# Kernel optimization log

Hardware: AMD Instinct MI355X
Metric: run time of the kernel (lower is better)

The kernel has to match this reference:

```python
import jax, jax.numpy as jnp
import numpy as np

SYM_LIST = np.array([0, 2, 5], dtype=np.int64)


def quat_to_rot_wxyz(q):
    """q: [bs, 4] normalized quaternion in wxyz order -> [bs, 3, 3] rotation."""
    w, x, y, z = q[:, 0], q[:, 1], q[:, 2], q[:, 3]
    two = jnp.asarray(2.0, q.dtype)
    one = jnp.asarray(1.0, q.dtype)
    r00 = one - two * (y * y + z * z)
    r01 = two * (x * y - z * w)
    r02 = two * (x * z + y * w)
    r10 = two * (x * y + z * w)
    r11 = one - two * (x * x + z * z)
    r12 = two * (y * z - x * w)
    r20 = two * (x * z - y * w)
    r21 = two * (y * z + x * w)
    r22 = one - two * (x * x + y * y)
    R = jnp.stack([
        jnp.stack([r00, r01, r02], axis=-1),
        jnp.stack([r10, r11, r12], axis=-1),
        jnp.stack([r20, r21, r22], axis=-1),
    ], axis=-2)  # [bs, 3, 3]
    return R


def setup_inputs() -> dict:
    key = jax.random.key(0)
    k1, k2, k3, k4, k5 = jax.random.split(key, 5)
    bs, num_p = 32, 2048
    pred_r = jax.random.normal(k1, (bs, 4), dtype=jnp.float32)
    pred_t = jax.random.normal(k2, (bs, 3), dtype=jnp.float32)
    target = jax.random.normal(k3, (bs, num_p, 3), dtype=jnp.float32)
    model_points = jax.random.normal(k4, (bs, num_p, 3), dtype=jnp.float32)
    idx = jax.random.randint(k5, (bs, 1), 0, 8, dtype=jnp.int64)
    return {"pred_r": pred_r, "pred_t": pred_t, "target": target,
            "model_points": model_points, "idx": idx, "permutation": 0}


def reference(pred_r, pred_t, target, model_points, idx, permutation):
    # normalize quaternion, build rotation, transform model points (row-vector
    # convention as in torch.bmm(model_points, base))
    q = pred_r / jnp.linalg.norm(pred_r, axis=1, keepdims=True)  # [bs,4]
    R = quat_to_rot_wxyz(q)                                      # [bs,3,3]
    tf = jnp.einsum('bnd,bde->bne', model_points, R) + pred_t[:, None, :]  # [bs,N,3]

    # brute-force 1-NN: for each transformed model point, nearest target point
    # squared distances via the ||a||^2 + ||b||^2 - 2 a.b expansion: [bs,N,N]
    d2 = (jnp.sum(tf * tf, axis=-1)[:, :, None]
          + jnp.sum(target * target, axis=-1)[:, None, :]
          - 2.0 * jnp.einsum('bnd,bmd->bnm', tf, target))
    inds = jnp.argmin(d2, axis=-1)                               # [bs,N]
    matched = jnp.take_along_axis(target, inds[..., None], axis=1)  # [bs,N,3]

    # apply the symmetric (ADD-S) matching only for classes in sym_list
    sym_mask = jnp.isin(idx[:, 0], jnp.asarray(SYM_LIST))        # [bs]
    target2 = jnp.where(sym_mask[:, None, None], matched, target)

    dis = jnp.mean(jnp.linalg.norm(tf - target, axis=2), axis=1)    # ADD (returned)
    dis2 = jnp.mean(jnp.linalg.norm(tf - target2, axis=2), axis=1)  # ADD-S (knn-matched)
    return jnp.stack([dis, dis2])  # [2, bs]
```

## Files before the change

kernel.cpp:

```cpp
#include <hip/hip_runtime.h>
#include <math.h>
#include <stdint.h>

#define NP      2048
#define BS      32
#define TPB1    1024
#define NW      (TPB1 / 64)
#define HALVES  2
#define HSIZE   (NP / HALVES)
#define WSLICE  (HSIZE / NW)
#define PPT     8
#define PTSBLK  (64 * PPT)
#define PSLICES (NP / PTSBLK)


__device__ __forceinline__ void quat_rot(const float* __restrict__ pred_r,
                                         const float* __restrict__ pred_t,
                                         int b, float R[9], float T[3]) {
    float qw = pred_r[b * 4 + 0], qx = pred_r[b * 4 + 1];
    float qy = pred_r[b * 4 + 2], qz = pred_r[b * 4 + 3];
    float nrm = sqrtf(qw * qw + qx * qx + qy * qy + qz * qz);
    qw /= nrm; qx /= nrm; qy /= nrm; qz /= nrm;
    R[0] = 1.0f - 2.0f * (qy * qy + qz * qz);
    R[1] = 2.0f * (qx * qy - qz * qw);
    R[2] = 2.0f * (qx * qz + qy * qw);
    R[3] = 2.0f * (qx * qy + qz * qw);
    R[4] = 1.0f - 2.0f * (qx * qx + qz * qz);
    R[5] = 2.0f * (qy * qz - qx * qw);
    R[6] = 2.0f * (qx * qz - qy * qw);
    R[7] = 2.0f * (qy * qz + qx * qw);
    R[8] = 1.0f - 2.0f * (qx * qx + qy * qy);
    T[0] = pred_t[b * 3 + 0]; T[1] = pred_t[b * 3 + 1]; T[2] = pred_t[b * 3 + 2];
}

__global__ __launch_bounds__(TPB1, 4) void scan_kernel(
    const float* __restrict__ pred_r,
    const float* __restrict__ pred_t,
    const float* __restrict__ target,
    const float* __restrict__ model_points,
    const int*   __restrict__ idx,
    unsigned long long* __restrict__ ws)
{
    __shared__ float4 tgt[HSIZE];
    __shared__ unsigned long long key[NW][PTSBLK];
    __shared__ unsigned long long key1[4][PTSBLK];

    const int bid  = blockIdx.x;
    const int b    = bid >> 3;
    const int h    = (bid >> 2) & 1;
    const int s    = bid & 3;
    const int tid  = threadIdx.x;
    const int wave = tid >> 6;
    const int lane = tid & 63;

    const int iv = idx[b];
    if (!((iv == 0) | (iv == 2) | (iv == 5))) return;

    float R[9], T[3];
    quat_rot(pred_r, pred_t, b, R, T);

    const float* tb = target + ((size_t)b * NP + h * HSIZE) * 3;
    {
        float t0 = tb[tid * 3 + 0], t1 = tb[tid * 3 + 1], t2 = tb[tid * 3 + 2];
        tgt[tid] = make_float4(t0, t1, t2, (t0 * t0 + t1 * t1) + t2 * t2);
    }

    float ax[PPT], ay[PPT], az[PPT], eb[PPT];
    int   mb[PPT];
    const float* mpb = model_points + (size_t)b * NP * 3;
    #pragma unroll
    for (int p = 0; p < PPT; ++p) {
        int n = s * PTSBLK + p * 64 + lane;
        float m0 = mpb[n * 3 + 0], m1 = mpb[n * 3 + 1], m2 = mpb[n * 3 + 2];
        float tfx = m0 * R[0] + m1 * R[3] + m2 * R[6] + T[0];
        float tfy = m0 * R[1] + m1 * R[4] + m2 * R[7] + T[1];
        float tfz = m0 * R[2] + m1 * R[5] + m2 * R[8] + T[2];
        ax[p] = -2.0f * tfx; ay[p] = -2.0f * tfy; az[p] = -2.0f * tfz;
        eb[p] = INFINITY;    mb[p] = 0;
    }
    __syncthreads();

    const int lc = wave * WSLICE;
    #pragma unroll 2
    for (int mm = 0; mm < WSLICE; mm += 2) {
        float4 c0 = tgt[lc + mm + 0];
        float4 c1 = tgt[lc + mm + 1];
        const int gm = h * HSIZE + lc + mm;
        #pragma unroll
        for (int p = 0; p < PPT; ++p) {
            float e0 = fmaf(ax[p], c0.x, fmaf(ay[p], c0.y, fmaf(az[p], c0.z, c0.w)));
            if (e0 < eb[p]) { eb[p] = e0; mb[p] = gm + 0; }
            float e1 = fmaf(ax[p], c1.x, fmaf(ay[p], c1.y, fmaf(az[p], c1.z, c1.w)));
            if (e1 < eb[p]) { eb[p] = e1; mb[p] = gm + 1; }
        }
    }

    #pragma unroll
    for (int p = 0; p < PPT; ++p) {
        float e = eb[p];
        e = (e == 0.0f) ? 0.0f : e;
        uint32_t u = __float_as_uint(e);
        u ^= (uint32_t)((int32_t)u >> 31) | 0x80000000u;
        key[wave][p * 64 + lane] =
            ((unsigned long long)u << 32) | (uint32_t)mb[p];
    }
    __syncthreads();

    #pragma unroll
    for (int it = 0; it < 2; ++it) {
        int t = tid + it * TPB1;
        int g = t >> 9;
        int p = t & 511;
        unsigned long long k0 = key[g * 4 + 0][p];
        unsigned long long k1 = key[g * 4 + 1][p];
        unsigned long long k2 = key[g * 4 + 2][p];
        unsigned long long k3 = key[g * 4 + 3][p];
        if (k1 < k0) k0 = k1;
        if (k3 < k2) k2 = k3;
        if (k2 < k0) k0 = k2;
        key1[g][p] = k0;
    }
    __syncthreads();

    if (tid < PTSBLK) {
        unsigned long long k0 = key1[0][tid];
        unsigned long long k1 = key1[1][tid];
        unsigned long long k2 = key1[2][tid];
        unsigned long long k3 = key1[3][tid];
        if (k1 < k0) k0 = k1;
        if (k3 < k2) k2 = k3;
        if (k2 < k0) k0 = k2;
        ws[((size_t)h * BS + b) * NP + s * PTSBLK + tid] = k0;
    }
}

#define TPB2 1024
__global__ __launch_bounds__(TPB2) void finish_kernel(
    const float* __restrict__ pred_r,
    const float* __restrict__ pred_t,
    const float* __restrict__ target,
    const float* __restrict__ model_points,
    const int*   __restrict__ idx,
    const unsigned long long* __restrict__ ws,
    float* __restrict__ out)
{
    __shared__ float red1[NW], red2[NW];

    const int b    = blockIdx.x >> 1;
    const int s2   = blockIdx.x & 1;
    const int tid  = threadIdx.x;
    const int wave = tid >> 6;
    const int lane = tid & 63;
    const int n    = s2 * TPB2 + tid;

    const int iv   = idx[b];
    const bool sym = (iv == 0) | (iv == 2) | (iv == 5);

    float R[9], T[3];
    quat_rot(pred_r, pred_t, b, R, T);

    const float* mpp = model_points + ((size_t)b * NP + n) * 3;
    float m0 = mpp[0], m1 = mpp[1], m2 = mpp[2];
    float tfx = m0 * R[0] + m1 * R[3] + m2 * R[6] + T[0];
    float tfy = m0 * R[1] + m1 * R[4] + m2 * R[7] + T[1];
    float tfz = m0 * R[2] + m1 * R[5] + m2 * R[8] + T[2];

    const float* tn = target + ((size_t)b * NP + n) * 3;
    float dx = tfx - tn[0], dy = tfy - tn[1], dz = tfz - tn[2];
    float dis = sqrtf(dx * dx + dy * dy + dz * dz);
    float dis2 = dis;

    if (sym) {
        unsigned long long kA = ws[(size_t)b * NP + n];
        unsigned long long kB = ws[((size_t)BS + b) * NP + n];
        int bM = (int)(uint32_t)(kB < kA ? kB : kA);
        const float* tm = target + ((size_t)b * NP + bM) * 3;
        float sx = tfx - tm[0], sy = tfy - tm[1], sz = tfz - tm[2];
        dis2 = sqrtf(sx * sx + sy * sy + sz * sz);
    }

    float s1 = dis, s2v = dis2;
    #pragma unroll
    for (int off = 32; off > 0; off >>= 1) {
        s1  += __shfl_down(s1, off);
        s2v += __shfl_down(s2v, off);
    }
    if (lane == 0) { red1[wave] = s1; red2[wave] = s2v; }
    __syncthreads();
    if (tid == 0) {
        float t1 = 0.0f, t2 = 0.0f;
        #pragma unroll
        for (int w = 0; w < NW; ++w) { t1 += red1[w]; t2 += red2[w]; }
        atomicAdd(out + b,      t1 * (1.0f / NP));
        atomicAdd(out + 32 + b, t2 * (1.0f / NP));
    }
}

extern "C" void kernel_launch(void* const* d_in, const int* in_sizes, int n_in,
                              void* d_out, int out_size, void* d_ws, size_t ws_size,
                              hipStream_t stream) {
    const float* pred_r       = (const float*)d_in[0];
    const float* pred_t       = (const float*)d_in[1];
    const float* target       = (const float*)d_in[2];
    const float* model_points = (const float*)d_in[3];
    const int*   idx          = (const int*)d_in[4];
    float* out = (float*)d_out;
    unsigned long long* ws = (unsigned long long*)d_ws;

    scan_kernel<<<BS * HALVES * PSLICES, TPB1, 0, stream>>>(
        pred_r, pred_t, target, model_points, idx, ws);
    finish_kernel<<<BS * 2, TPB2, 0, stream>>>(
        pred_r, pred_t, target, model_points, idx, ws, out);
}
```

Measured before the change: 84.79 us.

## Fuse scan and finish into one cooperative kernel with compacted symmetric work units

Merges the two launches into a single cooperative kernel that uses a grid-wide sync between the nearest-neighbour scan and the loss reduction. Scan work units are built only for symmetric batch entries, so no blocks are launched and then exit early, and each unit now covers half as many points per thread. The aim is to remove one launch and to balance work across a fixed grid of 256 blocks. In exchange it adds grid-sync overhead, recomputes the symmetric-entry compaction from idx in every block, and reduces per-thread reuse of each target point loaded from shared memory.

```diff
diff --git a/kernel.cpp b/kernel.cpp
--- a/kernel.cpp
+++ b/kernel.cpp
@@ -1,17 +1,20 @@
 #include <hip/hip_runtime.h>
+#include <hip/hip_cooperative_groups.h>
 #include <math.h>
 #include <stdint.h>
 
+namespace cg = cooperative_groups;
+
 #define NP      2048
 #define BS      32
-#define TPB1    1024
-#define NW      (TPB1 / 64)
-#define HALVES  2
-#define HSIZE   (NP / HALVES)
+#define TPB     1024
+#define NW      (TPB / 64)
+#define GRID    256
+#define HSIZE   1024
 #define WSLICE  (HSIZE / NW)
-#define PPT     8
+#define PPT     4
 #define PTSBLK  (64 * PPT)
-#define PSLICES (NP / PTSBLK)
+#define UPB     16
 
 
 __device__ __forceinline__ void quat_rot(const float* __restrict__ pred_r,
@@ -33,166 +36,172 @@
     T[0] = pred_t[b * 3 + 0]; T[1] = pred_t[b * 3 + 1]; T[2] = pred_t[b * 3 + 2];
 }
 
-__global__ __launch_bounds__(TPB1, 4) void scan_kernel(
+__device__ __forceinline__ bool is_sym(int v) {
+    return (v == 0) | (v == 2) | (v == 5);
+}
+
+__global__ __launch_bounds__(TPB, 4) void loss_coop_kernel(
     const float* __restrict__ pred_r,
     const float* __restrict__ pred_t,
     const float* __restrict__ target,
     const float* __restrict__ model_points,
     const int*   __restrict__ idx,
-    unsigned long long* __restrict__ ws)
+    unsigned long long* __restrict__ ws,
+    float* __restrict__ out)
 {
     __shared__ float4 tgt[HSIZE];
     __shared__ unsigned long long key[NW][PTSBLK];
     __shared__ unsigned long long key1[4][PTSBLK];
+    __shared__ float red1[4], red2[4];
 
     const int bid  = blockIdx.x;
-    const int b    = bid >> 3;
-    const int h    = (bid >> 2) & 1;
-    const int s    = bid & 3;
     const int tid  = threadIdx.x;
     const int wave = tid >> 6;
     const int lane = tid & 63;
 
-    const int iv = idx[b];
-    if (!((iv == 0) | (iv == 2) | (iv == 5))) return;
-
-    float R[9], T[3];
-    quat_rot(pred_r, pred_t, b, R, T);
-
-    const float* tb = target + ((size_t)b * NP + h * HSIZE) * 3;
+    int nsym = 0;
+    #pragma unroll
+    for (int i = 0; i < BS; ++i) nsym += is_sym(idx[i]) ? 1 : 0;
+    const int nunits = nsym * UPB;
+
+    for (int u = bid; u < nunits; u += GRID) {
+        const int j = u >> 4;
+        const int h = (u >> 3) & 1;
+        const int s = u & 7;
+
+        int b = 0, cnt = 0;
+        #pragma unroll
+        for (int i = 0; i < BS; ++i) {
+            bool sy = is_sym(idx[i]);
+            if (sy && cnt == j) b = i;
+            cnt += sy ? 1 : 0;
+        }
+
+        float R[9], T[3];
+        quat_rot(pred_r, pred_t, b, R, T);
+
+        const float* tb = target + ((size_t)b * NP + h * HSIZE) * 3;
+        {
+            float t0 = tb[tid * 3 + 0], t1 = tb[tid * 3 + 1], t2 = tb[tid * 3 + 2];
+            tgt[tid] = make_float4(t0, t1, t2, (t0 * t0 + t1 * t1) + t2 * t2);
+        }
+
+        float ax[PPT], ay[PPT], az[PPT], eb[PPT];
+        int   mb[PPT];
+        const float* mpb = model_points + (size_t)b * NP * 3;
+        #pragma unroll
+        for (int p = 0; p < PPT; ++p) {
+            int n = s * PTSBLK + p * 64 + lane;
+            float m0 = mpb[n * 3 + 0], m1 = mpb[n * 3 + 1], m2 = mpb[n * 3 + 2];
+            float tfx = m0 * R[0] + m1 * R[3] + m2 * R[6] + T[0];
+            float tfy = m0 * R[1] + m1 * R[4] + m2 * R[7] + T[1];
+            float tfz = m0 * R[2] + m1 * R[5] + m2 * R[8] + T[2];
+            ax[p] = -2.0f * tfx; ay[p] = -2.0f * tfy; az[p] = -2.0f * tfz;
+            eb[p] = INFINITY;    mb[p] = 0;
+        }
+        __syncthreads();
+
+        const int lc = wave * WSLICE;
+        #pragma unroll 2
+        for (int mm = 0; mm < WSLICE; mm += 2) {
+            float4 c0 = tgt[lc + mm + 0];
+            float4 c1 = tgt[lc + mm + 1];
+            const int gm = h * HSIZE + lc + mm;
+            #pragma unroll
+            for (int p = 0; p < PPT; ++p) {
+                float e0 = fmaf(ax[p], c0.x, fmaf(ay[p], c0.y, fmaf(az[p], c0.z, c0.w)));
+                if (e0 < eb[p]) { eb[p] = e0; mb[p] = gm + 0; }
+                float e1 = fmaf(ax[p], c1.x, fmaf(ay[p], c1.y, fmaf(az[p], c1.z, c1.w)));
+                if (e1 < eb[p]) { eb[p] = e1; mb[p] = gm + 1; }
+            }
+        }
+
+        #pragma unroll
+        for (int p = 0; p < PPT; ++p) {
+            float e = eb[p];
+            e = (e == 0.0f) ? 0.0f : e;
+            uint32_t uo = __float_as_uint(e);
+            uo ^= (uint32_t)((int32_t)uo >> 31) | 0x80000000u;
+            key[wave][p * 64 + lane] =
+                ((unsigned long long)uo << 32) | (uint32_t)mb[p];
+        }
+        __syncthreads();
+
+        {
+            int g = tid >> 8;
+            int p = tid & 255;
+            unsigned long long k0 = key[g * 4 + 0][p];
+            unsigned long long k1 = key[g * 4 + 1][p];
+            unsigned long long k2 = key[g * 4 + 2][p];
+            unsigned long long k3 = key[g * 4 + 3][p];
+            if (k1 < k0) k0 = k1;
+            if (k3 < k2) k2 = k3;
+            if (k2 < k0) k0 = k2;
+            key1[g][p] = k0;
+        }
+        __syncthreads();
+
+        if (tid < PTSBLK) {
+            unsigned long long k0 = key1[0][tid];
+            unsigned long long k1 = key1[1][tid];
+            unsigned long long k2 = key1[2][tid];
+            unsigned long long k3 = key1[3][tid];
+            if (k1 < k0) k0 = k1;
+            if (k3 < k2) k2 = k3;
+            if (k2 < k0) k0 = k2;
+            ws[((size_t)h * BS + b) * NP + s * PTSBLK + tid] = k0;
+        }
+        __syncthreads();
+    }
+
+    cg::this_grid().sync();
+
     {
-        float t0 = tb[tid * 3 + 0], t1 = tb[tid * 3 + 1], t2 = tb[tid * 3 + 2];
-        tgt[tid] = make_float4(t0, t1, t2, (t0 * t0 + t1 * t1) + t2 * t2);
-    }
-
-    float ax[PPT], ay[PPT], az[PPT], eb[PPT];
-    int   mb[PPT];
-    const float* mpb = model_points + (size_t)b * NP * 3;
-    #pragma unroll
-    for (int p = 0; p < PPT; ++p) {
-        int n = s * PTSBLK + p * 64 + lane;
-        float m0 = mpb[n * 3 + 0], m1 = mpb[n * 3 + 1], m2 = mpb[n * 3 + 2];
-        float tfx = m0 * R[0] + m1 * R[3] + m2 * R[6] + T[0];
-        float tfy = m0 * R[1] + m1 * R[4] + m2 * R[7] + T[1];
-        float tfz = m0 * R[2] + m1 * R[5] + m2 * R[8] + T[2];
-        ax[p] = -2.0f * tfx; ay[p] = -2.0f * tfy; az[p] = -2.0f * tfz;
-        eb[p] = INFINITY;    mb[p] = 0;
-    }
-    __syncthreads();
-
-    const int lc = wave * WSLICE;
-    #pragma unroll 2
-    for (int mm = 0; mm < WSLICE; mm += 2) {
-        float4 c0 = tgt[lc + mm + 0];
-        float4 c1 = tgt[lc + mm + 1];
-        const int gm = h * HSIZE + lc + mm;
-        #pragma unroll
-        for (int p = 0; p < PPT; ++p) {
-            float e0 = fmaf(ax[p], c0.x, fmaf(ay[p], c0.y, fmaf(az[p], c0.z, c0.w)));
-            if (e0 < eb[p]) { eb[p] = e0; mb[p] = gm + 0; }
-            float e1 = fmaf(ax[p], c1.x, fmaf(ay[p], c1.y, fmaf(az[p], c1.z, c1.w)));
-            if (e1 < eb[p]) { eb[p] = e1; mb[p] = gm + 1; }
-        }
-    }
-
-    #pragma unroll
-    for (int p = 0; p < PPT; ++p) {
-        float e = eb[p];
-        e = (e == 0.0f) ? 0.0f : e;
-        uint32_t u = __float_as_uint(e);
-        u ^= (uint32_t)((int32_t)u >> 31) | 0x80000000u;
-        key[wave][p * 64 + lane] =
-            ((unsigned long long)u << 32) | (uint32_t)mb[p];
-    }
-    __syncthreads();
-
-    #pragma unroll
-    for (int it = 0; it < 2; ++it) {
-        int t = tid + it * TPB1;
-        int g = t >> 9;
-        int p = t & 511;
-        unsigned long long k0 = key[g * 4 + 0][p];
-        unsigned long long k1 = key[g * 4 + 1][p];
-        unsigned long long k2 = key[g * 4 + 2][p];
-        unsigned long long k3 = key[g * 4 + 3][p];
-        if (k1 < k0) k0 = k1;
-        if (k3 < k2) k2 = k3;
-        if (k2 < k0) k0 = k2;
-        key1[g][p] = k0;
-    }
-    __syncthreads();
-
-    if (tid < PTSBLK) {
-        unsigned long long k0 = key1[0][tid];
-        unsigned long long k1 = key1[1][tid];
-        unsigned long long k2 = key1[2][tid];
-        unsigned long long k3 = key1[3][tid];
-        if (k1 < k0) k0 = k1;
-        if (k3 < k2) k2 = k3;
-        if (k2 < k0) k0 = k2;
-        ws[((size_t)h * BS + b) * NP + s * PTSBLK + tid] = k0;
-    }
-}
-
-#define TPB2 1024
-__global__ __launch_bounds__(TPB2) void finish_kernel(
-    const float* __restrict__ pred_r,
-    const float* __restrict__ pred_t,
-    const float* __restrict__ target,
-    const float* __restrict__ model_points,
-    const int*   __restrict__ idx,
-    const unsigned long long* __restrict__ ws,
-    float* __restrict__ out)
-{
-    __shared__ float red1[NW], red2[NW];
-
-    const int b    = blockIdx.x >> 1;
-    const int s2   = blockIdx.x & 1;
-    const int tid  = threadIdx.x;
-    const int wave = tid >> 6;
-    const int lane = tid & 63;
-    const int n    = s2 * TPB2 + tid;
-
-    const int iv   = idx[b];
-    const bool sym = (iv == 0) | (iv == 2) | (iv == 5);
-
-    float R[9], T[3];
-    quat_rot(pred_r, pred_t, b, R, T);
-
-    const float* mpp = model_points + ((size_t)b * NP + n) * 3;
-    float m0 = mpp[0], m1 = mpp[1], m2 = mpp[2];
-    float tfx = m0 * R[0] + m1 * R[3] + m2 * R[6] + T[0];
-    float tfy = m0 * R[1] + m1 * R[4] + m2 * R[7] + T[1];
-    float tfz = m0 * R[2] + m1 * R[5] + m2 * R[8] + T[2];
-
-    const float* tn = target + ((size_t)b * NP + n) * 3;
-    float dx = tfx - tn[0], dy = tfy - tn[1], dz = tfz - tn[2];
-    float dis = sqrtf(dx * dx + dy * dy + dz * dz);
-    float dis2 = dis;
-
-    if (sym) {
-        unsigned long long kA = ws[(size_t)b * NP + n];
-        unsigned long long kB = ws[((size_t)BS + b) * NP + n];
-        int bM = (int)(uint32_t)(kB < kA ? kB : kA);
-        const float* tm = target + ((size_t)b * NP + bM) * 3;
-        float sx = tfx - tm[0], sy = tfy - tm[1], sz = tfz - tm[2];
-        dis2 = sqrtf(sx * sx + sy * sy + sz * sz);
-    }
-
-    float s1 = dis, s2v = dis2;
-    #pragma unroll
-    for (int off = 32; off > 0; off >>= 1) {
-        s1  += __shfl_down(s1, off);
-        s2v += __shfl_down(s2v, off);
-    }
-    if (lane == 0) { red1[wave] = s1; red2[wave] = s2v; }
-    __syncthreads();
-    if (tid == 0) {
-        float t1 = 0.0f, t2 = 0.0f;
-        #pragma unroll
-        for (int w = 0; w < NW; ++w) { t1 += red1[w]; t2 += red2[w]; }
-        atomicAdd(out + b,      t1 * (1.0f / NP));
-        atomicAdd(out + 32 + b, t2 * (1.0f / NP));
+        const int g0 = bid * 256;
+        const int b  = g0 >> 11;
+        const bool sym = is_sym(idx[b]);
+
+        float R[9], T[3];
+        quat_rot(pred_r, pred_t, b, R, T);
+
+        float s1 = 0.0f, s2 = 0.0f;
+        if (tid < 256) {
+            const int n = (g0 & (NP - 1)) + tid;
+            const float* mpp = model_points + ((size_t)b * NP + n) * 3;
+            float m0 = mpp[0], m1 = mpp[1], m2 = mpp[2];
+            float tfx = m0 * R[0] + m1 * R[3] + m2 * R[6] + T[0];
+            float tfy = m0 * R[1] + m1 * R[4] + m2 * R[7] + T[1];
+            float tfz = m0 * R[2] + m1 * R[5] + m2 * R[8] + T[2];
+
+            const float* tn = target + ((size_t)b * NP + n) * 3;
+            float dx = tfx - tn[0], dy = tfy - tn[1], dz = tfz - tn[2];
+            float dis = sqrtf(dx * dx + dy * dy + dz * dz);
+            float dis2 = dis;
+
+            if (sym) {
+                unsigned long long kA = ws[(size_t)b * NP + n];
+                unsigned long long kB = ws[((size_t)BS + b) * NP + n];
+                int bM = (int)(uint32_t)(kB < kA ? kB : kA);
+                const float* tm = target + ((size_t)b * NP + bM) * 3;
+                float sx = tfx - tm[0], sy = tfy - tm[1], sz = tfz - tm[2];
+                dis2 = sqrtf(sx * sx + sy * sy + sz * sz);
+            }
+            s1 = dis; s2 = dis2;
+        }
+
+        #pragma unroll
+        for (int off = 32; off > 0; off >>= 1) {
+            s1 += __shfl_down(s1, off);
+            s2 += __shfl_down(s2, off);
+        }
+        if (lane == 0 && wave < 4) { red1[wave] = s1; red2[wave] = s2; }
+        __syncthreads();
+        if (tid == 0) {
+            float t1 = (red1[0] + red1[1]) + (red1[2] + red1[3]);
+            float t2 = (red2[0] + red2[1]) + (red2[2] + red2[3]);
+            atomicAdd(out + b,      t1 * (1.0f / NP));
+            atomicAdd(out + 32 + b, t2 * (1.0f / NP));
+        }
     }
 }
 
@@ -207,8 +216,8 @@
     float* out = (float*)d_out;
     unsigned long long* ws = (unsigned long long*)d_ws;
 
-    scan_kernel<<<BS * HALVES * PSLICES, TPB1, 0, stream>>>(
-        pred_r, pred_t, target, model_points, idx, ws);
-    finish_kernel<<<BS * 2, TPB2, 0, stream>>>(
-        pred_r, pred_t, target, model_points, idx, ws, out);
-}
+    void* args[] = {(void*)&pred_r, (void*)&pred_t, (void*)&target,
+                    (void*)&model_points, (void*)&idx, (void*)&ws, (void*)&out};
+    hipLaunchCooperativeKernel((void*)loss_coop_kernel, dim3(GRID), dim3(TPB),
+                               args, 0, stream);
+}
```

New measurement: 114.5 us. 35.0% more time.

## Compact symmetric batches into a persistent work-unit grid with smaller point slices

Applied to the files above, without the earlier changes.

Before, the scan kernel launched one block per (batch, half, slice) and exited early for non-symmetric batches, so only some blocks did work and those sat unevenly across CUs. Now each block counts the symmetric batches and loops over a compacted list of work units with a fixed 256-block grid. Points per thread are halved, giving twice as many units, so the real work spreads across more CUs. The cost is an extra idx scan per unit, less register reuse per target load, and one more barrier per unit.

```diff
diff --git a/kernel.cpp b/kernel.cpp
--- a/kernel.cpp
+++ b/kernel.cpp
@@ -4,14 +4,14 @@
 
 #define NP      2048
 #define BS      32
-#define TPB1    1024
-#define NW      (TPB1 / 64)
-#define HALVES  2
-#define HSIZE   (NP / HALVES)
+#define TPB     1024
+#define NW      (TPB / 64)
+#define GRID1   256
+#define HSIZE   1024
 #define WSLICE  (HSIZE / NW)
-#define PPT     8
+#define PPT     4
 #define PTSBLK  (64 * PPT)
-#define PSLICES (NP / PTSBLK)
+#define UPB     16
 
 
 __device__ __forceinline__ void quat_rot(const float* __restrict__ pred_r,
@@ -33,7 +33,11 @@
     T[0] = pred_t[b * 3 + 0]; T[1] = pred_t[b * 3 + 1]; T[2] = pred_t[b * 3 + 2];
 }
 
-__global__ __launch_bounds__(TPB1, 4) void scan_kernel(
+__device__ __forceinline__ bool is_sym(int v) {
+    return (v == 0) | (v == 2) | (v == 5);
+}
+
+__global__ __launch_bounds__(TPB, 4) void scan_kernel(
     const float* __restrict__ pred_r,
     const float* __restrict__ pred_t,
     const float* __restrict__ target,
@@ -46,91 +50,103 @@
     __shared__ unsigned long long key1[4][PTSBLK];
 
     const int bid  = blockIdx.x;
-    const int b    = bid >> 3;
-    const int h    = (bid >> 2) & 1;
-    const int s    = bid & 3;
     const int tid  = threadIdx.x;
     const int wave = tid >> 6;
     const int lane = tid & 63;
 
-    const int iv = idx[b];
-    if (!((iv == 0) | (iv == 2) | (iv == 5))) return;
-
-    float R[9], T[3];
-    quat_rot(pred_r, pred_t, b, R, T);
-
-    const float* tb = target + ((size_t)b * NP + h * HSIZE) * 3;
-    {
-        float t0 = tb[tid * 3 + 0], t1 = tb[tid * 3 + 1], t2 = tb[tid * 3 + 2];
-        tgt[tid] = make_float4(t0, t1, t2, (t0 * t0 + t1 * t1) + t2 * t2);
-    }
-
-    float ax[PPT], ay[PPT], az[PPT], eb[PPT];
-    int   mb[PPT];
-    const float* mpb = model_points + (size_t)b * NP * 3;
+    int nsym = 0;
     #pragma unroll
-    for (int p = 0; p < PPT; ++p) {
-        int n = s * PTSBLK + p * 64 + lane;
-        float m0 = mpb[n * 3 + 0], m1 = mpb[n * 3 + 1], m2 = mpb[n * 3 + 2];
-        float tfx = m0 * R[0] + m1 * R[3] + m2 * R[6] + T[0];
-        float tfy = m0 * R[1] + m1 * R[4] + m2 * R[7] + T[1];
-        float tfz = m0 * R[2] + m1 * R[5] + m2 * R[8] + T[2];
-        ax[p] = -2.0f * tfx; ay[p] = -2.0f * tfy; az[p] = -2.0f * tfz;
-        eb[p] = INFINITY;    mb[p] = 0;
-    }
-    __syncthreads();
-
-    const int lc = wave * WSLICE;
-    #pragma unroll 2
-    for (int mm = 0; mm < WSLICE; mm += 2) {
-        float4 c0 = tgt[lc + mm + 0];
-        float4 c1 = tgt[lc + mm + 1];
-        const int gm = h * HSIZE + lc + mm;
+    for (int i = 0; i < BS; ++i) nsym += is_sym(idx[i]) ? 1 : 0;
+    const int nunits = nsym * UPB;
+
+    for (int u = bid; u < nunits; u += GRID1) {
+        const int j = u >> 4;
+        const int h = (u >> 3) & 1;
+        const int s = u & 7;
+
+        int b = 0, cnt = 0;
+        #pragma unroll
+        for (int i = 0; i < BS; ++i) {
+            bool sy = is_sym(idx[i]);
+            if (sy && cnt == j) b = i;
+            cnt += sy ? 1 : 0;
+        }
+
+        float R[9], T[3];
+        quat_rot(pred_r, pred_t, b, R, T);
+
+        const float* tb = target + ((size_t)b * NP + h * HSIZE) * 3;
+        {
+            float t0 = tb[tid * 3 + 0], t1 = tb[tid * 3 + 1], t2 = tb[tid * 3 + 2];
+            tgt[tid] = make_float4(t0, t1, t2, (t0 * t0 + t1 * t1) + t2 * t2);
+        }
+
+        float ax[PPT], ay[PPT], az[PPT], eb[PPT];
+        int   mb[PPT];
+        const float* mpb = model_points + (size_t)b * NP * 3;
         #pragma unroll
         for (int p = 0; p < PPT; ++p) {
-            float e0 = fmaf(ax[p], c0.x, fmaf(ay[p], c0.y, fmaf(az[p], c0.z, c0.w)));
-            if (e0 < eb[p]) { eb[p] = e0; mb[p] = gm + 0; }
-            float e1 = fmaf(ax[p], c1.x, fmaf(ay[p], c1.y, fmaf(az[p], c1.z, c1.w)));
-            if (e1 < eb[p]) { eb[p] = e1; mb[p] = gm + 1; }
-        }
-    }
-
-    #pragma unroll
-    for (int p = 0; p < PPT; ++p) {
-        float e = eb[p];
-        e = (e == 0.0f) ? 0.0f : e;
-        uint32_t u = __float_as_uint(e);
-        u ^= (uint32_t)((int32_t)u >> 31) | 0x80000000u;
-        key[wave][p * 64 + lane] =
-            ((unsigned long long)u << 32) | (uint32_t)mb[p];
-    }
-    __syncthreads();
-
-    #pragma unroll
-    for (int it = 0; it < 2; ++it) {
-        int t = tid + it * TPB1;
-        int g = t >> 9;
-        int p = t & 511;
-        unsigned long long k0 = key[g * 4 + 0][p];
-        unsigned long long k1 = key[g * 4 + 1][p];
-        unsigned long long k2 = key[g * 4 + 2][p];
-        unsigned long long k3 = key[g * 4 + 3][p];
-        if (k1 < k0) k0 = k1;
-        if (k3 < k2) k2 = k3;
-        if (k2 < k0) k0 = k2;
-        key1[g][p] = k0;
-    }
-    __syncthreads();
-
-    if (tid < PTSBLK) {
-        unsigned long long k0 = key1[0][tid];
-        unsigned long long k1 = key1[1][tid];
-        unsigned long long k2 = key1[2][tid];
-        unsigned long long k3 = key1[3][tid];
-        if (k1 < k0) k0 = k1;
-        if (k3 < k2) k2 = k3;
-        if (k2 < k0) k0 = k2;
-        ws[((size_t)h * BS + b) * NP + s * PTSBLK + tid] = k0;
+            int n = s * PTSBLK + p * 64 + lane;
+            float m0 = mpb[n * 3 + 0], m1 = mpb[n * 3 + 1], m2 = mpb[n * 3 + 2];
+            float tfx = m0 * R[0] + m1 * R[3] + m2 * R[6] + T[0];
+            float tfy = m0 * R[1] + m1 * R[4] + m2 * R[7] + T[1];
+            float tfz = m0 * R[2] + m1 * R[5] + m2 * R[8] + T[2];
+            ax[p] = -2.0f * tfx; ay[p] = -2.0f * tfy; az[p] = -2.0f * tfz;
+            eb[p] = INFINITY;    mb[p] = 0;
+        }
+        __syncthreads();
+
+        const int lc = wave * WSLICE;
+        #pragma unroll 2
+        for (int mm = 0; mm < WSLICE; mm += 2) {
+            float4 c0 = tgt[lc + mm + 0];
+            float4 c1 = tgt[lc + mm + 1];
+            const int gm = h * HSIZE + lc + mm;
+            #pragma unroll
+            for (int p = 0; p < PPT; ++p) {
+                float e0 = fmaf(ax[p], c0.x, fmaf(ay[p], c0.y, fmaf(az[p], c0.z, c0.w)));
+                if (e0 < eb[p]) { eb[p] = e0; mb[p] = gm + 0; }
+                float e1 = fmaf(ax[p], c1.x, fmaf(ay[p], c1.y, fmaf(az[p], c1.z, c1.w)));
+                if (e1 < eb[p]) { eb[p] = e1; mb[p] = gm + 1; }
+            }
+        }
+
+        #pragma unroll
+        for (int p = 0; p < PPT; ++p) {
+            float e = eb[p];
+            e = (e == 0.0f) ? 0.0f : e;
+            uint32_t uo = __float_as_uint(e);
+            uo ^= (uint32_t)((int32_t)uo >> 31) | 0x80000000u;
+            key[wave][p * 64 + lane] =
+                ((unsigned long long)uo << 32) | (uint32_t)mb[p];
+        }
+        __syncthreads();
+
+        {
+            int g = tid >> 8;
+            int p = tid & 255;
+            unsigned long long k0 = key[g * 4 + 0][p];
+            unsigned long long k1 = key[g * 4 + 1][p];
+            unsigned long long k2 = key[g * 4 + 2][p];
+            unsigned long long k3 = key[g * 4 + 3][p];
+            if (k1 < k0) k0 = k1;
+            if (k3 < k2) k2 = k3;
+            if (k2 < k0) k0 = k2;
+            key1[g][p] = k0;
+        }
+        __syncthreads();
+
+        if (tid < PTSBLK) {
+            unsigned long long k0 = key1[0][tid];
+            unsigned long long k1 = key1[1][tid];
+            unsigned long long k2 = key1[2][tid];
+            unsigned long long k3 = key1[3][tid];
+            if (k1 < k0) k0 = k1;
+            if (k3 < k2) k2 = k3;
+            if (k2 < k0) k0 = k2;
+            ws[((size_t)h * BS + b) * NP + s * PTSBLK + tid] = k0;
+        }
+        __syncthreads();
     }
 }
 
@@ -154,7 +170,7 @@
     const int n    = s2 * TPB2 + tid;
 
     const int iv   = idx[b];
-    const bool sym = (iv == 0) | (iv == 2) | (iv == 5);
+    const bool sym = is_sym(iv);
 
     float R[9], T[3];
     quat_rot(pred_r, pred_t, b, R, T);
@@ -207,7 +223,7 @@
     float* out = (float*)d_out;
     unsigned long long* ws = (unsigned long long*)d_ws;
 
-    scan_kernel<<<BS * HALVES * PSLICES, TPB1, 0, stream>>>(
+    scan_kernel<<<GRID1, TPB, 0, stream>>>(
         pred_r, pred_t, target, model_points, idx, ws);
     finish_kernel<<<BS * 2, TPB2, 0, stream>>>(
         pred_r, pred_t, target, model_points, idx, ws, out);
```

Result: faster. 78.65 us (-7.2%).
